# Kernel tuning notes

Measured on AMD Instinct MI355X. Metric: run time of the kernel, lower is better.

Reference implementation:

```python
import jax, jax.numpy as jnp
import numpy as np

N_HEADS = 8
D_EMBED = 512
D_HEAD = D_EMBED // N_HEADS


def setup_inputs() -> dict:
    key = jax.random.key(0)
    ks = jax.random.split(key, 5)
    B, S, D = 8, 2048, D_EMBED
    scale_in = 1.0 / np.sqrt(D)
    x = jax.random.normal(ks[0], (B, S, D), dtype=jnp.float32)
    # torch nn.Linear weights: (out_features, in_features)
    w_in = jax.random.normal(ks[1], (3 * D, D), dtype=jnp.float32) * scale_in
    b_in = jax.random.normal(ks[2], (3 * D,), dtype=jnp.float32) * scale_in
    w_out = jax.random.normal(ks[3], (D, D), dtype=jnp.float32) * scale_in
    b_out = jax.random.normal(ks[4], (D,), dtype=jnp.float32) * scale_in
    return {"x": x, "w_in": w_in, "b_in": b_in, "w_out": w_out, "b_out": b_out}


def reference(x, w_in, b_in, w_out, b_out):
    B, S, D = x.shape
    H, Dh = N_HEADS, D_HEAD
    # fused QKV projection (torch Linear: x @ W^T + b)
    qkv = x @ w_in.T + b_in                     # (B, S, 3D)
    q, k, v = jnp.split(qkv, 3, axis=-1)        # each (B, S, D)
    # split heads -> (B, H, S, Dh)
    def heads(t):
        return t.reshape(B, S, H, Dh).transpose(0, 2, 1, 3)
    q, k, v = heads(q), heads(k), heads(v)
    # scaled dot-product attention (full matrix, as in source)
    scores = jnp.einsum("bhqd,bhkd->bhqk", q, k) / jnp.sqrt(jnp.float32(Dh))
    weights = jax.nn.softmax(scores, axis=-1)   # (B, H, S, S)
    out = jnp.einsum("bhqk,bhkd->bhqd", weights, v)
    out = out.transpose(0, 2, 1, 3).reshape(B, S, D)
    return out @ w_out.T + b_out
```

## Files before the change

### kernel.cpp

```cpp
#include <hip/hip_runtime.h>
#include <stdint.h>

#define SEQ   2048
#define DEMB  512
#define NH    8
#define DH    64
#define BATCH 8
#define M_ROWS (BATCH * SEQ)
#define QKLD  1024
#define QSCALE 0.18033688011112042f

typedef __attribute__((ext_vector_type(8))) __bf16 bf16x8;
typedef __attribute__((ext_vector_type(4))) __bf16 bf16x4;
typedef __attribute__((ext_vector_type(4))) float  f32x4;
typedef __attribute__((ext_vector_type(8))) uint16_t u16x8;
typedef __attribute__((ext_vector_type(4))) uint32_t u32x4;

__device__ __forceinline__ void gll16(const __bf16* g, __bf16* l) {
    __builtin_amdgcn_global_load_lds(
        (__attribute__((address_space(1))) void*)(__bf16*)g,
        (__attribute__((address_space(3))) void*)l, 16, 0, 0);
}

__device__ __forceinline__ bf16x8 ld8(const __bf16* p) {
    return *(const bf16x8*)p;
}

__device__ __forceinline__ uint32_t pkpair(float a, float b) {
    const uint16_t lo = __builtin_bit_cast(uint16_t, (__bf16)a);
    const uint16_t hi = __builtin_bit_cast(uint16_t, (__bf16)b);
    return (uint32_t)lo | ((uint32_t)hi << 16);
}

__device__ __forceinline__ int sw(int row, int chunk) {
    return row * 64 + ((chunk ^ (row & 7)) << 3);
}

__device__ __forceinline__ void stage_gll_sw(const __bf16* g, int gld,
                                             __bf16* l, int wave, int lane) {
    const int lr = lane >> 3;
    const int scol = ((lane & 7) ^ lr) * 8;
    #pragma unroll
    for (int i = 0; i < 2; i++) {
        const int r0 = i * 32 + wave * 8;
        gll16(g + (size_t)(r0 + lr) * gld + scol, l + r0 * 64);
    }
}

__device__ __forceinline__ void stage_gll(const __bf16* src, __bf16* dst,
                                          int ld, int wave, int lane) {
    const int srow = lane >> 3, scol = (lane & 7) * 8;
    #pragma unroll
    for (int i = 0; i < 4; i++) {
        const int r0 = (i * 4 + wave) * 8;
        gll16(src + (size_t)(r0 + srow) * ld + scol, dst + r0 * 64);
    }
}

#define NXQ (M_ROWS * DEMB / 4)
#define NWQ (3 * DEMB * DEMB / 4)
#define NOQ (DEMB * DEMB / 4)

__global__ __launch_bounds__(256)
void cvt_all(const float* __restrict__ x, const float* __restrict__ w_in,
             __bf16* __restrict__ xb, __bf16* __restrict__ wb) {
    const int i = blockIdx.x * 256 + threadIdx.x;
    const float4* src;
    bf16x4* dst;
    if (i < NXQ) { src = (const float4*)x + i;         dst = (bf16x4*)xb + i; }
    else if (i < NXQ + NWQ) {
        const int j = i - NXQ;
        src = (const float4*)w_in + j;  dst = (bf16x4*)wb + j;
    } else return;
    const float4 v = *src;
    bf16x4 b;
    b[0] = (__bf16)v.x; b[1] = (__bf16)v.y;
    b[2] = (__bf16)v.z; b[3] = (__bf16)v.w;
    *dst = b;
}

__global__ __launch_bounds__(256)
void cvt_wout(const float* __restrict__ w, __bf16* __restrict__ wb) {
    const int i = blockIdx.x * 256 + threadIdx.x;
    if (i < NOQ) {
        const float4 v = ((const float4*)w)[i];
        bf16x4 b;
        b[0] = (__bf16)v.x; b[1] = (__bf16)v.y;
        b[2] = (__bf16)v.z; b[3] = (__bf16)v.w;
        ((bf16x4*)wb)[i] = b;
    }
}

__global__ __launch_bounds__(256)
void gemm_qkv(const __bf16* __restrict__ A, const __bf16* __restrict__ W,
              const float* __restrict__ bias, __bf16* __restrict__ qk,
              __bf16* __restrict__ vt) {
    constexpr int K = DEMB;
    __shared__ __align__(16) __bf16 SM[128 * 128];
    __bf16* As = SM;
    __bf16* Bs = SM + 128 * 64;

    const int tid  = threadIdx.x;
    const int wave = tid >> 6, lane = tid & 63;
    const int quad = lane >> 4, l16 = lane & 15;
    const int m0 = blockIdx.x * 128, n0 = blockIdx.y * 128;
    const int wm = wave & 1, wn = wave >> 1;
    const bool qkblk = (n0 < QKLD);

    f32x4 acc[4][4] = {};

    for (int k0 = 0; k0 < K; k0 += 64) {
        __syncthreads();
        stage_gll(A + (size_t)m0 * K + k0, As, K, wave, lane);
        stage_gll(W + (size_t)n0 * K + k0, Bs, K, wave, lane);
        __syncthreads();
        #pragma unroll
        for (int ks = 0; ks < 2; ks++) {
            bf16x8 af[4], bf[4];
            #pragma unroll
            for (int t = 0; t < 4; t++) {
                af[t] = ld8(&As[(wm * 64 + t * 16 + l16) * 64 + ks * 32 + quad * 8]);
                bf[t] = ld8(&Bs[(wn * 64 + t * 16 + l16) * 64 + ks * 32 + quad * 8]);
            }
            if (qkblk) {
                #pragma unroll
                for (int j = 0; j < 4; j++)
                    #pragma unroll
                    for (int i = 0; i < 4; i++)
                        acc[j][i] = __builtin_amdgcn_mfma_f32_16x16x32_bf16(
                            bf[j], af[i], acc[j][i], 0, 0, 0);
            } else {
                #pragma unroll
                for (int i = 0; i < 4; i++)
                    #pragma unroll
                    for (int j = 0; j < 4; j++)
                        acc[i][j] = __builtin_amdgcn_mfma_f32_16x16x32_bf16(
                            af[i], bf[j], acc[i][j], 0, 0, 0);
            }
        }
    }

    __syncthreads();

    if (qkblk) {
        const float scl = (n0 < DEMB) ? QSCALE : 1.0f;
        #pragma unroll
        for (int j = 0; j < 4; j++) {
            const int nl = wn * 64 + j * 16 + quad * 4;
            const float4 bv4 = *(const float4*)&bias[n0 + nl];
            const int chunk = nl >> 3;
            #pragma unroll
            for (int i = 0; i < 4; i++) {
                const int ml = wm * 64 + i * 16 + l16;
                bf16x4 pk;
                pk[0] = (__bf16)((acc[j][i][0] + bv4.x) * scl);
                pk[1] = (__bf16)((acc[j][i][1] + bv4.y) * scl);
                pk[2] = (__bf16)((acc[j][i][2] + bv4.z) * scl);
                pk[3] = (__bf16)((acc[j][i][3] + bv4.w) * scl);
                const int phys = ((chunk & 7) ^ (ml & 7)) | (chunk & 8);
                *(bf16x4*)(&SM[ml * 128 + phys * 8 + (nl & 7)]) = pk;
            }
        }
        __syncthreads();
        const int g = tid >> 4, li = tid & 15;
        #pragma unroll
        for (int it = 0; it < 8; it++) {
            const int row = it * 16 + g;
            const int phys = ((li & 7) ^ (row & 7)) | (li & 8);
            bf16x8 v = ld8(&SM[row * 128 + phys * 8]);
            *(bf16x8*)(qk + (size_t)(m0 + row) * QKLD + n0 + li * 8) = v;
        }
    } else {
        const int hd0 = n0 - QKLD;
        const int bb = m0 >> 11, s0 = m0 & (SEQ - 1);
        #pragma unroll
        for (int j = 0; j < 4; j++) {
            const int n = n0 + wn * 64 + j * 16 + l16;
            const float bv = bias[n];
            const int hdl = wn * 64 + j * 16 + l16;
            #pragma unroll
            for (int i = 0; i < 4; i++) {
                const int sl = wm * 64 + i * 16 + quad * 4;
                bf16x4 pk;
                #pragma unroll
                for (int r = 0; r < 4; r++)
                    pk[r] = (__bf16)(acc[i][j][r] + bv);
                const int chunk = sl >> 3;
                const int phys = (((chunk & 7) ^ (hdl & 7)) | (chunk & 8));
                *(bf16x4*)(&SM[hdl * 128 + phys * 8 + (sl & 7)]) = pk;
            }
        }
        __syncthreads();
        const int g = tid >> 4, li = tid & 15;
        #pragma unroll
        for (int it = 0; it < 8; it++) {
            const int row = it * 16 + g;
            const int phys = (((li & 7) ^ (row & 7)) | (li & 8));
            bf16x8 v = ld8(&SM[row * 128 + phys * 8]);
            *(bf16x8*)(vt + ((size_t)(bb * DEMB + hd0 + row)) * SEQ + s0 + li * 8) = v;
        }
    }
}

__global__ __launch_bounds__(256, 4)
void attn_flash(const __bf16* __restrict__ qk, const __bf16* __restrict__ vt,
                __bf16* __restrict__ outp) {
    const int qt = blockIdx.x, h = blockIdx.y, b = blockIdx.z;
    const int tid  = threadIdx.x;
    const int wave = tid >> 6, lane = tid & 63;
    const int quad = lane >> 4, l16 = lane & 15;

    __shared__ __align__(16) __bf16 Ks[2][64 * 64];
    __shared__ __align__(16) __bf16 Vt[2][64 * 64];

    const size_t brow = (size_t)b * SEQ;
    const int q0 = qt * 128 + wave * 32;
    const __bf16* kbase = qk + brow * QKLD + DEMB + h * DH;
    const __bf16* vbase = vt + ((size_t)(b * DEMB + h * DH)) * SEQ;

    const u16x8 one16 = {0x3F80, 0x3F80, 0x3F80, 0x3F80,
                         0x3F80, 0x3F80, 0x3F80, 0x3F80};
    const bf16x8 ONES = __builtin_bit_cast(bf16x8, one16);

    bf16x8 qf[2][2];
    #pragma unroll
    for (int qb = 0; qb < 2; qb++) {
        const __bf16* qp = qk + (brow + q0 + qb * 16 + l16) * QKLD + h * DH + quad * 8;
        qf[qb][0] = ld8(qp);
        qf[qb][1] = ld8(qp + 32);
    }

    f32x4 o[2][4] = {};
    f32x4 osum[2] = {};

    stage_gll_sw(kbase, QKLD, Ks[0], wave, lane);
    stage_gll_sw(vbase, SEQ,  Vt[0], wave, lane);

    for (int t = 0; t < SEQ / 64; t++) {
        __syncthreads();
        if (t + 1 < SEQ / 64) {
            const int nb = (t + 1) & 1;
            stage_gll_sw(kbase + (size_t)(t + 1) * 64 * QKLD, QKLD, Ks[nb], wave, lane);
            stage_gll_sw(vbase + (t + 1) * 64,                SEQ,  Vt[nb], wave, lane);
        }
        const int buf = t & 1;

        uint32_t pk[2][4][2];
        __builtin_amdgcn_s_setprio(1);
        #pragma unroll
        for (int kt = 0; kt < 4; kt++) {
            bf16x8 kf0 = ld8(&Ks[buf][sw(kt * 16 + l16, quad)]);
            bf16x8 kf1 = ld8(&Ks[buf][sw(kt * 16 + l16, 4 + quad)]);
            #pragma unroll
            for (int qb = 0; qb < 2; qb++) {
                f32x4 c = {};
                c = __builtin_amdgcn_mfma_f32_16x16x32_bf16(kf0, qf[qb][0], c, 0, 0, 0);
                c = __builtin_amdgcn_mfma_f32_16x16x32_bf16(kf1, qf[qb][1], c, 0, 0, 0);
                pk[qb][kt][0] = pkpair(__builtin_amdgcn_exp2f(c[0]),
                                       __builtin_amdgcn_exp2f(c[1]));
                pk[qb][kt][1] = pkpair(__builtin_amdgcn_exp2f(c[2]),
                                       __builtin_amdgcn_exp2f(c[3]));
            }
        }
        __builtin_amdgcn_s_setprio(0);

        bf16x8 pf[2][2];
        #pragma unroll
        for (int qb = 0; qb < 2; qb++) {
            #pragma unroll
            for (int f = 0; f < 2; f++) {
                uint32_t a0 = pk[qb][2 * f][0], b0 = pk[qb][2 * f + 1][0];
                uint32_t a1 = pk[qb][2 * f][1], b1 = pk[qb][2 * f + 1][1];
                {
                    auto r = __builtin_amdgcn_permlane32_swap(a0, b0, false, false);
                    a0 = r[0]; b0 = r[1];
                }
                {
                    auto r = __builtin_amdgcn_permlane32_swap(a1, b1, false, false);
                    a1 = r[0]; b1 = r[1];
                }
                {
                    auto r = __builtin_amdgcn_permlane16_swap(a0, b0, false, false);
                    a0 = r[0]; b0 = r[1];
                }
                {
                    auto r = __builtin_amdgcn_permlane16_swap(a1, b1, false, false);
                    a1 = r[0]; b1 = r[1];
                }
                u32x4 d;
                d[0] = a0; d[1] = a1; d[2] = b0; d[3] = b1;
                pf[qb][f] = __builtin_bit_cast(bf16x8, d);
            }
            osum[qb] = __builtin_amdgcn_mfma_f32_16x16x32_bf16(pf[qb][0], ONES, osum[qb], 0, 0, 0);
            osum[qb] = __builtin_amdgcn_mfma_f32_16x16x32_bf16(pf[qb][1], ONES, osum[qb], 0, 0, 0);
        }

        __builtin_amdgcn_s_setprio(1);
        #pragma unroll
        for (int db = 0; db < 4; db++) {
            bf16x8 vf0 = ld8(&Vt[buf][sw(db * 16 + l16, quad)]);
            bf16x8 vf1 = ld8(&Vt[buf][sw(db * 16 + l16, 4 + quad)]);
            #pragma unroll
            for (int qb = 0; qb < 2; qb++) {
                o[qb][db] = __builtin_amdgcn_mfma_f32_16x16x32_bf16(pf[qb][0], vf0, o[qb][db], 0, 0, 0);
                o[qb][db] = __builtin_amdgcn_mfma_f32_16x16x32_bf16(pf[qb][1], vf1, o[qb][db], 0, 0, 0);
            }
        }
        __builtin_amdgcn_s_setprio(0);
    }

    #pragma unroll
    for (int qb = 0; qb < 2; qb++)
        #pragma unroll
        for (int r = 0; r < 4; r++) {
            const float linv = __builtin_amdgcn_rcpf(osum[qb][r]);
            const int q = q0 + qb * 16 + quad * 4 + r;
            #pragma unroll
            for (int db = 0; db < 4; db++)
                outp[(brow + q) * DEMB + h * DH + db * 16 + l16] =
                    (__bf16)(o[qb][db][r] * linv);
        }
}

__global__ __launch_bounds__(256)
void gemm_out(const __bf16* __restrict__ A, const __bf16* __restrict__ W,
              const float* __restrict__ bias, float* __restrict__ C,
              int N, int K) {
    __shared__ __align__(16) __bf16 SMO[2 * 128 * 64];
    __bf16* As = SMO;
    __bf16* Bs = SMO + 128 * 64;

    const int tid  = threadIdx.x;
    const int wave = tid >> 6, lane = tid & 63;
    const int quad = lane >> 4, l16 = lane & 15;
    const int m0 = blockIdx.x * 128, n0 = blockIdx.y * 128;
    const int wm = wave & 1, wn = wave >> 1;

    f32x4 acc[4][4] = {};

    for (int k0 = 0; k0 < K; k0 += 64) {
        __syncthreads();
        stage_gll(A + (size_t)m0 * K + k0, As, K, wave, lane);
        stage_gll(W + (size_t)n0 * K + k0, Bs, K, wave, lane);
        __syncthreads();
        #pragma unroll
        for (int ks = 0; ks < 2; ks++) {
            bf16x8 af[4], bf[4];
            #pragma unroll
            for (int t = 0; t < 4; t++) {
                af[t] = ld8(&As[(wm * 64 + t * 16 + l16) * 64 + ks * 32 + quad * 8]);
                bf[t] = ld8(&Bs[(wn * 64 + t * 16 + l16) * 64 + ks * 32 + quad * 8]);
            }
            #pragma unroll
            for (int j = 0; j < 4; j++)
                #pragma unroll
                for (int i = 0; i < 4; i++)
                    acc[j][i] = __builtin_amdgcn_mfma_f32_16x16x32_bf16(
                        bf[j], af[i], acc[j][i], 0, 0, 0);
        }
    }

    __syncthreads();
    float* SMf = (float*)SMO;

    #pragma unroll
    for (int p = 0; p < 2; p++) {
        if (p) __syncthreads();
        if (wm == p) {
            #pragma unroll
            for (int j = 0; j < 4; j++) {
                const int nl = wn * 64 + j * 16 + quad * 4;
                const float4 bv4 = *(const float4*)&bias[n0 + nl];
                const int chunkf = nl >> 2;
                #pragma unroll
                for (int i = 0; i < 4; i++) {
                    const int ml = i * 16 + l16;
                    const int physf = ((chunkf & 7) ^ (ml & 7)) | (chunkf & 24);
                    float4 v;
                    v.x = acc[j][i][0] + bv4.x;
                    v.y = acc[j][i][1] + bv4.y;
                    v.z = acc[j][i][2] + bv4.z;
                    v.w = acc[j][i][3] + bv4.w;
                    *(float4*)(&SMf[ml * 128 + physf * 4]) = v;
                }
            }
        }
        __syncthreads();
        const int g2 = tid >> 5, li2 = tid & 31;
        #pragma unroll
        for (int it = 0; it < 8; it++) {
            const int row = it * 8 + g2;
            const int physf = ((li2 & 7) ^ (row & 7)) | (li2 & 24);
            float4 v = *(const float4*)&SMf[row * 128 + physf * 4];
            *(float4*)(&C[(size_t)(m0 + p * 64 + row) * N + n0 + li2 * 4]) = v;
        }
    }
}

extern "C" void kernel_launch(void* const* d_in, const int* in_sizes, int n_in,
                              void* d_out, int out_size, void* d_ws, size_t ws_size,
                              hipStream_t stream) {
    const float* x     = (const float*)d_in[0];
    const float* w_in  = (const float*)d_in[1];
    const float* b_in  = (const float*)d_in[2];
    const float* w_out = (const float*)d_in[3];
    const float* b_out = (const float*)d_in[4];

    __bf16* qk   = (__bf16*)d_ws;
    __bf16* vtb  = qk + (size_t)M_ROWS * QKLD;
    __bf16* xbuf = vtb + (size_t)BATCH * DEMB * SEQ;
    __bf16* aout = xbuf;
    __bf16* woutb = vtb;
    __bf16* winb = (__bf16*)((char*)d_out + 24u * 1024 * 1024);
    float*  outp = (float*)d_out;

    cvt_all<<<(NXQ + NWQ + 255) / 256, 256, 0, stream>>>(x, w_in, xbuf, winb);
    gemm_qkv<<<dim3(M_ROWS / 128, 12), 256, 0, stream>>>(xbuf, winb, b_in, qk, vtb);
    attn_flash<<<dim3(SEQ / 128, NH, BATCH), 256, 0, stream>>>(qk, vtb, aout);
    cvt_wout<<<NOQ / 256, 256, 0, stream>>>(w_out, woutb);
    gemm_out<<<dim3(M_ROWS / 128, DEMB / 128), 256, 0, stream>>>(
        aout, woutb, b_out, outp, DEMB, DEMB);
}
```

Measured before the change: 233.4 us.

## Software-pipeline attention loop so QK of next tile overlaps softmax and PV

Restructures the flash attention inner loop so the QK^T scores for tile t+1 are computed alongside the PV product of tile t, with exp/softmax of the held scores done in between. K tiles are prefetched two steps ahead and V one step ahead to match the new schedule. The aim is to let MFMA work overlap the exp/permlane softmax stage instead of serialising the three phases. Keeping the scores live raises register pressure, so launch bounds drop from 4 to 3 blocks per SM, lowering occupancy.

```diff
diff --git a/kernel.cpp b/kernel.cpp
--- a/kernel.cpp
+++ b/kernel.cpp
@@ -202,7 +202,7 @@
     }
 }
 
-__global__ __launch_bounds__(256, 4)
+__global__ __launch_bounds__(256, 3)
 void attn_flash(const __bf16* __restrict__ qk, const __bf16* __restrict__ vt,
                 __bf16* __restrict__ outp) {
     const int qt = blockIdx.x, h = blockIdx.y, b = blockIdx.z;
@@ -232,45 +232,40 @@
 
     f32x4 o[2][4] = {};
     f32x4 osum[2] = {};
-
-    stage_gll_sw(kbase, QKLD, Ks[0], wave, lane);
-    stage_gll_sw(vbase, SEQ,  Vt[0], wave, lane);
-
-    for (int t = 0; t < SEQ / 64; t++) {
-        __syncthreads();
-        if (t + 1 < SEQ / 64) {
-            const int nb = (t + 1) & 1;
-            stage_gll_sw(kbase + (size_t)(t + 1) * 64 * QKLD, QKLD, Ks[nb], wave, lane);
-            stage_gll_sw(vbase + (t + 1) * 64,                SEQ,  Vt[nb], wave, lane);
-        }
-        const int buf = t & 1;
-
-        uint32_t pk[2][4][2];
-        __builtin_amdgcn_s_setprio(1);
+    f32x4 st[2][4];
+    bf16x8 pf[2][2];
+
+    auto do_qk = [&](int tt) {
+        const int bufq = tt & 1;
         #pragma unroll
         for (int kt = 0; kt < 4; kt++) {
-            bf16x8 kf0 = ld8(&Ks[buf][sw(kt * 16 + l16, quad)]);
-            bf16x8 kf1 = ld8(&Ks[buf][sw(kt * 16 + l16, 4 + quad)]);
+            bf16x8 kf0 = ld8(&Ks[bufq][sw(kt * 16 + l16, quad)]);
+            bf16x8 kf1 = ld8(&Ks[bufq][sw(kt * 16 + l16, 4 + quad)]);
             #pragma unroll
             for (int qb = 0; qb < 2; qb++) {
                 f32x4 c = {};
                 c = __builtin_amdgcn_mfma_f32_16x16x32_bf16(kf0, qf[qb][0], c, 0, 0, 0);
                 c = __builtin_amdgcn_mfma_f32_16x16x32_bf16(kf1, qf[qb][1], c, 0, 0, 0);
-                pk[qb][kt][0] = pkpair(__builtin_amdgcn_exp2f(c[0]),
-                                       __builtin_amdgcn_exp2f(c[1]));
-                pk[qb][kt][1] = pkpair(__builtin_amdgcn_exp2f(c[2]),
-                                       __builtin_amdgcn_exp2f(c[3]));
-            }
-        }
-        __builtin_amdgcn_s_setprio(0);
-
-        bf16x8 pf[2][2];
+                st[qb][kt] = c;
+            }
+        }
+    };
+
+    auto do_softmax = [&]() {
         #pragma unroll
         for (int qb = 0; qb < 2; qb++) {
+            uint32_t pk[4][2];
+            #pragma unroll
+            for (int kt = 0; kt < 4; kt++) {
+                pk[kt][0] = pkpair(__builtin_amdgcn_exp2f(st[qb][kt][0]),
+                                   __builtin_amdgcn_exp2f(st[qb][kt][1]));
+                pk[kt][1] = pkpair(__builtin_amdgcn_exp2f(st[qb][kt][2]),
+                                   __builtin_amdgcn_exp2f(st[qb][kt][3]));
+            }
             #pragma unroll
             for (int f = 0; f < 2; f++) {
-                uint32_t a0 = pk[qb][2 * f][0], b0 = pk[qb][2 * f + 1][0];
-                uint32_t a1 = pk[qb][2 * f][1], b1 = pk[qb][2 * f + 1][1];
+                uint32_t a0 = pk[2 * f][0], b0 = pk[2 * f + 1][0];
+                uint32_t a1 = pk[2 * f][1], b1 = pk[2 * f + 1][1];
                 {
                     auto r = __builtin_amdgcn_permlane32_swap(a0, b0, false, false);
                     a0 = r[0]; b0 = r[1];
@@ -294,20 +289,46 @@
             osum[qb] = __builtin_amdgcn_mfma_f32_16x16x32_bf16(pf[qb][0], ONES, osum[qb], 0, 0, 0);
             osum[qb] = __builtin_amdgcn_mfma_f32_16x16x32_bf16(pf[qb][1], ONES, osum[qb], 0, 0, 0);
         }
-
-        __builtin_amdgcn_s_setprio(1);
+    };
+
+    auto do_pv = [&](int tt) {
+        const int bufv = tt & 1;
         #pragma unroll
         for (int db = 0; db < 4; db++) {
-            bf16x8 vf0 = ld8(&Vt[buf][sw(db * 16 + l16, quad)]);
-            bf16x8 vf1 = ld8(&Vt[buf][sw(db * 16 + l16, 4 + quad)]);
+            bf16x8 vf0 = ld8(&Vt[bufv][sw(db * 16 + l16, quad)]);
+            bf16x8 vf1 = ld8(&Vt[bufv][sw(db * 16 + l16, 4 + quad)]);
             #pragma unroll
             for (int qb = 0; qb < 2; qb++) {
                 o[qb][db] = __builtin_amdgcn_mfma_f32_16x16x32_bf16(pf[qb][0], vf0, o[qb][db], 0, 0, 0);
                 o[qb][db] = __builtin_amdgcn_mfma_f32_16x16x32_bf16(pf[qb][1], vf1, o[qb][db], 0, 0, 0);
             }
         }
+    };
+
+    constexpr int NT = SEQ / 64;
+
+    stage_gll_sw(kbase,                      QKLD, Ks[0], wave, lane);
+    stage_gll_sw(vbase,                      SEQ,  Vt[0], wave, lane);
+    stage_gll_sw(kbase + (size_t)64 * QKLD,  QKLD, Ks[1], wave, lane);
+    __syncthreads();
+    do_qk(0);
+
+    for (int t = 0; t < NT - 1; ++t) {
+        __syncthreads();
+        if (t + 2 < NT)
+            stage_gll_sw(kbase + (size_t)(t + 2) * 64 * QKLD, QKLD, Ks[t & 1], wave, lane);
+        stage_gll_sw(vbase + (t + 1) * 64, SEQ, Vt[(t + 1) & 1], wave, lane);
+
+        do_softmax();
+        __builtin_amdgcn_s_setprio(1);
+        do_qk(t + 1);
+        do_pv(t);
         __builtin_amdgcn_s_setprio(0);
     }
+
+    __syncthreads();
+    do_softmax();
+    do_pv(NT - 1);
 
     #pragma unroll
     for (int qb = 0; qb < 2; qb++)
```

Result: no change. 230.0 us (-1.5%).
